# Performance work log

Measured on AMD Instinct MI355X. Metric: run time of the kernel, lower is better.

The kernel has to match this reference:

```python
import jax, jax.numpy as jnp
import numpy as np

N = 32768       # total nodes = NUM_GRAPHS * T
F_IN = 32       # num_features
HC = 64         # hidden_channels
HEADS = 4
E = 524288      # edges before self-loops
NUM_GRAPHS = 64 # == batch.max()+1 by construction
T = 512         # time steps per graph (N // NUM_GRAPHS)
OUT = 24        # output_size
NEG_SLOPE = 0.2 # PyG GATConv default


def gat_layer(x, src, dst, W, a_src, a_dst, b, n_nodes):
    """PyG GATConv (concat=True) with edge softmax over incoming edges."""
    H, C = a_src.shape
    h = (x @ W).reshape(n_nodes, H, C)                    # [N,H,C]
    alpha_src = jnp.sum(h * a_src, axis=-1)               # [N,H]
    alpha_dst = jnp.sum(h * a_dst, axis=-1)               # [N,H]
    e = jax.nn.leaky_relu(alpha_src[src] + alpha_dst[dst], NEG_SLOPE)  # [E,H]
    m = jax.ops.segment_max(e, dst, num_segments=n_nodes)
    e = jnp.exp(e - m[dst])
    s = jax.ops.segment_sum(e, dst, num_segments=n_nodes)
    alpha = e / (s[dst] + 1e-16)                          # [E,H]
    msg = h[src] * alpha[..., None]                       # [E,H,C]
    out = jax.ops.segment_sum(msg, dst, num_segments=n_nodes)  # [N,H,C]
    return out.reshape(n_nodes, H * C) + b


def gru_layer(x, Wih, Whh, bih, bhh):
    """torch nn.GRU single layer, batch_first input x: [B,T,Hin] -> ([B,T,H], h_T)."""
    Bsz = x.shape[0]
    H = Whh.shape[1]

    def step(h, xt):
        gi = xt @ Wih.T + bih
        gh = h @ Whh.T + bhh
        ir, iz, inn = jnp.split(gi, 3, axis=-1)
        hr, hz, hn = jnp.split(gh, 3, axis=-1)
        r = jax.nn.sigmoid(ir + hr)
        z = jax.nn.sigmoid(iz + hz)
        n = jnp.tanh(inn + r * hn)
        h_new = (1.0 - z) * n + z * h
        return h_new, h_new

    h0 = jnp.zeros((Bsz, H), x.dtype)
    hT, ys = jax.lax.scan(step, h0, jnp.swapaxes(x, 0, 1))
    return jnp.swapaxes(ys, 0, 1), hT


def setup_inputs() -> dict:
    key = jax.random.key(0)
    ks = jax.random.split(key, 24)
    sc = 0.1
    inp = {
        "x": jax.random.normal(ks[0], (N, F_IN), dtype=jnp.float32),
        "edge_index": jax.random.randint(ks[1], (2, E), 0, N, dtype=jnp.int32),
        "batch": jnp.repeat(jnp.arange(NUM_GRAPHS, dtype=jnp.int32), T),
        # GAT layer 1: F_IN -> HC x HEADS (concat)
        "W1": sc * jax.random.normal(ks[2], (F_IN, HEADS * HC), dtype=jnp.float32),
        "a_src1": sc * jax.random.normal(ks[3], (HEADS, HC), dtype=jnp.float32),
        "a_dst1": sc * jax.random.normal(ks[4], (HEADS, HC), dtype=jnp.float32),
        "b1": jnp.zeros((HEADS * HC,), dtype=jnp.float32),
        # GAT layer 2: HEADS*HC -> HC, 1 head
        "W2": sc * jax.random.normal(ks[5], (HEADS * HC, HC), dtype=jnp.float32),
        "a_src2": sc * jax.random.normal(ks[6], (1, HC), dtype=jnp.float32),
        "a_dst2": sc * jax.random.normal(ks[7], (1, HC), dtype=jnp.float32),
        "b2": jnp.zeros((HC,), dtype=jnp.float32),
        # GRU (2 layers, input_size == hidden_size == HC)
        "gru_Wih0": sc * jax.random.normal(ks[8], (3 * HC, HC), dtype=jnp.float32),
        "gru_Whh0": sc * jax.random.normal(ks[9], (3 * HC, HC), dtype=jnp.float32),
        "gru_bih0": jnp.zeros((3 * HC,), dtype=jnp.float32),
        "gru_bhh0": jnp.zeros((3 * HC,), dtype=jnp.float32),
        "gru_Wih1": sc * jax.random.normal(ks[10], (3 * HC, HC), dtype=jnp.float32),
        "gru_Whh1": sc * jax.random.normal(ks[11], (3 * HC, HC), dtype=jnp.float32),
        "gru_bih1": jnp.zeros((3 * HC,), dtype=jnp.float32),
        "gru_bhh1": jnp.zeros((3 * HC,), dtype=jnp.float32),
        # Linear head
        "Wl": sc * jax.random.normal(ks[12], (OUT, HC), dtype=jnp.float32),
        "bl": jnp.zeros((OUT,), dtype=jnp.float32),
    }
    return inp


def reference(x, edge_index, batch, W1, a_src1, a_dst1, b1, W2, a_src2, a_dst2, b2,
              gru_Wih0, gru_Whh0, gru_bih0, gru_bhh0,
              gru_Wih1, gru_Whh1, gru_bih1, gru_bhh1, Wl, bl):
    # PyG GATConv default add_self_loops=True
    loops = jnp.arange(N, dtype=edge_index.dtype)
    src = jnp.concatenate([edge_index[0], loops])
    dst = jnp.concatenate([edge_index[1], loops])

    h = jax.nn.elu(gat_layer(x, src, dst, W1, a_src1, a_dst1, b1, N))   # [N, HEADS*HC]
    h = jax.nn.elu(gat_layer(h, src, dst, W2, a_src2, a_dst2, b2, N))   # [N, HC]

    # batch is repeat(arange(NUM_GRAPHS), T) so batch.max()+1 == NUM_GRAPHS (static)
    seq = h.reshape(NUM_GRAPHS, T, HC)
    seq, _ = gru_layer(seq, gru_Wih0, gru_Whh0, gru_bih0, gru_bhh0)
    _, hT = gru_layer(seq, gru_Wih1, gru_Whh1, gru_bih1, gru_bhh1)      # [B, HC]
    return hT @ Wl.T + bl                                               # [B, OUT]
```

## Files before the change

### kernel.cpp

```cpp
#include <hip/hip_runtime.h>
#include <hip/hip_bf16.h>

#define N_NODES 32768
#define F_IN    32
#define HC      64
#define HEADS   4
#define NE      524288
#define NET     (NE + N_NODES)
#define NG      64
#define TT      512
#define OUTF    24

__device__ __forceinline__ float lrelu(float x){ return x > 0.f ? x : 0.2f*x; }
__device__ __forceinline__ float eluf (float x){ return x > 0.f ? x : __expf(x)-1.f; }
__device__ __forceinline__ float sigmf(float x){ return 1.f/(1.f+__expf(-x)); }
__device__ __forceinline__ float tanhfast(float x){ return 1.f - 2.f/(__expf(2.f*x)+1.f); }
__device__ __forceinline__ float bcast(float v, int k){
  return __int_as_float(__builtin_amdgcn_readlane(__float_as_int(v), k));
}

__global__ __launch_bounds__(256) void k_deg(const int* __restrict__ ei,
                                             int* __restrict__ deg){
  int e = blockIdx.x*256 + threadIdx.x;
  int d = (e < NE) ? ei[NE+e] : (e - NE);
  atomicAdd(deg + d, 1);
}

__global__ __launch_bounds__(1024) void k_scan(const int* __restrict__ deg,
                                               int* __restrict__ rowptr){
  __shared__ int ps[1024];
  const int t = threadIdx.x;
  const int base = t*32;
  int local[32]; int s = 0;
  #pragma unroll
  for(int i=0;i<32;i++){ local[i]=deg[base+i]; s+=local[i]; }
  ps[t]=s; __syncthreads();
  for(int off=1; off<1024; off<<=1){
    int v = (t>=off) ? ps[t-off] : 0;
    __syncthreads();
    ps[t]+=v;
    __syncthreads();
  }
  int run = (t==0) ? 0 : ps[t-1];
  #pragma unroll
  for(int i=0;i<32;i++){ rowptr[base+i]=run; run+=local[i]; }
  if(t==1023) rowptr[N_NODES]=run;
}

__global__ __launch_bounds__(256) void k_fill(const int* __restrict__ ei,
                                              const int* __restrict__ rowptr,
                                              int* __restrict__ cur,
                                              int* __restrict__ col){
  int e = blockIdx.x*256 + threadIdx.x;
  int s, d;
  if(e < NE){ s = ei[e]; d = ei[NE+e]; } else { s = e-NE; d = s; }
  int pos = atomicAdd(cur + d, 1);
  col[rowptr[d] + pos] = s;
}

__global__ __launch_bounds__(256) void k_alpha1x(const float* __restrict__ x,
                                                 const float* __restrict__ W1,
                                                 const float* __restrict__ a_src,
                                                 const float* __restrict__ a_dst,
                                                 float* __restrict__ as1,
                                                 float* __restrict__ ad1){
  __shared__ float ps[256];
  const int tid = threadIdx.x;
  {
    const int k = tid>>3, q = tid&7;
    const int h = q>>1, isd = q&1;
    const float* av = (isd ? a_dst : a_src) + h*64;
    const float* wr = W1 + k*256 + h*64;
    float acc = 0.f;
    #pragma unroll
    for(int c=0;c<64;c++) acc += wr[c]*av[c];
    ps[(isd?128:0) + k*4 + h] = acc;
  }
  __syncthreads();
  const int n = blockIdx.x*256 + tid;
  const float4* xr = (const float4*)(x + n*32);
  float sa0=0.f,sa1=0.f,sa2=0.f,sa3=0.f, sd0=0.f,sd1=0.f,sd2=0.f,sd3=0.f;
  #pragma unroll
  for(int k4=0;k4<8;k4++){
    float4 v = xr[k4];
    const float* pa = ps + (4*k4)*4;
    const float* pd = ps + 128 + (4*k4)*4;
    sa0 += v.x*pa[0] + v.y*pa[4] + v.z*pa[8]  + v.w*pa[12];
    sa1 += v.x*pa[1] + v.y*pa[5] + v.z*pa[9]  + v.w*pa[13];
    sa2 += v.x*pa[2] + v.y*pa[6] + v.z*pa[10] + v.w*pa[14];
    sa3 += v.x*pa[3] + v.y*pa[7] + v.z*pa[11] + v.w*pa[15];
    sd0 += v.x*pd[0] + v.y*pd[4] + v.z*pd[8]  + v.w*pd[12];
    sd1 += v.x*pd[1] + v.y*pd[5] + v.z*pd[9]  + v.w*pd[13];
    sd2 += v.x*pd[2] + v.y*pd[6] + v.z*pd[10] + v.w*pd[14];
    sd3 += v.x*pd[3] + v.y*pd[7] + v.z*pd[11] + v.w*pd[15];
  }
  *(float4*)(as1+n*4) = make_float4(sa0,sa1,sa2,sa3);
  *(float4*)(ad1+n*4) = make_float4(sd0,sd1,sd2,sd3);
}

__global__ __launch_bounds__(256) void k_gatx(const int* __restrict__ rowptr,
                                              const int* __restrict__ col,
                                              const float* __restrict__ as1,
                                              const float* __restrict__ ad1,
                                              const float* __restrict__ x,
                                              float* __restrict__ agg,
                                              float* __restrict__ s14){
  const int node = blockIdx.x*4 + (threadIdx.x>>6);
  const int lane = threadIdx.x & 63;
  const int h0   = lane>>5;
  const int c    = lane & 31;
  const int beg = rowptr[node], end = rowptr[node+1];
  const float adA = ad1[node*4 + h0];
  const float adB = ad1[node*4 + h0 + 2];
  float accA=0.f, accB=0.f, wsA=0.f, wsB=0.f;
  int j = beg;
  for(; j+3 < end; j += 4){
    int s0 = col[j], s1 = col[j+1], s2 = col[j+2], s3 = col[j+3];
    float4 q0 = *(const float4*)(as1 + s0*4);
    float4 q1 = *(const float4*)(as1 + s1*4);
    float4 q2 = *(const float4*)(as1 + s2*4);
    float4 q3 = *(const float4*)(as1 + s3*4);
    float x0 = x[s0*32 + c];
    float x1 = x[s1*32 + c];
    float x2 = x[s2*32 + c];
    float x3 = x[s3*32 + c];
    float wA0 = __expf(lrelu((h0?q0.y:q0.x) + adA));
    float wA1 = __expf(lrelu((h0?q1.y:q1.x) + adA));
    float wA2 = __expf(lrelu((h0?q2.y:q2.x) + adA));
    float wA3 = __expf(lrelu((h0?q3.y:q3.x) + adA));
    float wB0 = __expf(lrelu((h0?q0.w:q0.z) + adB));
    float wB1 = __expf(lrelu((h0?q1.w:q1.z) + adB));
    float wB2 = __expf(lrelu((h0?q2.w:q2.z) + adB));
    float wB3 = __expf(lrelu((h0?q3.w:q3.z) + adB));
    accA += wA0*x0 + wA1*x1 + wA2*x2 + wA3*x3;
    accB += wB0*x0 + wB1*x1 + wB2*x2 + wB3*x3;
    wsA  += (wA0+wA1) + (wA2+wA3);
    wsB  += (wB0+wB1) + (wB2+wB3);
  }
  for(; j < end; j++){
    int s0 = col[j];
    float4 q0 = *(const float4*)(as1 + s0*4);
    float wA0 = __expf(lrelu((h0?q0.y:q0.x) + adA));
    float wB0 = __expf(lrelu((h0?q0.w:q0.z) + adB));
    float x0 = x[s0*32 + c];
    accA += wA0*x0; accB += wB0*x0;
    wsA += wA0; wsB += wB0;
  }
  agg[node*128 + h0*32 + c]     = accA;
  agg[node*128 + (h0+2)*32 + c] = accB;
  if(c == 0){
    s14[node*4 + h0]     = wsA;
    s14[node*4 + h0 + 2] = wsB;
  }
}

__global__ __launch_bounds__(256) void k_g12(const float* __restrict__ agg,
                                             const float* __restrict__ W1,
                                             const float* __restrict__ s14,
                                             const float* __restrict__ b1,
                                             const float* __restrict__ W2,
                                             const float* __restrict__ a_src2,
                                             const float* __restrict__ a_dst2,
                                             float* __restrict__ h2,
                                             float* __restrict__ as2,
                                             float* __restrict__ ad2){
  __shared__ __align__(16) float ags[32*128];
  __shared__ __align__(16) float o1s[32*256];
  __shared__ float sv[128];
  const int tid  = threadIdx.x;
  const int row0 = blockIdx.x*32;
  const float4* ag = (const float4*)(agg + (size_t)row0*128);
  float4* a4 = (float4*)ags;
  for(int i=tid;i<1024;i+=256) a4[i]=ag[i];
  if(tid<32) ((float4*)sv)[tid]=((const float4*)(s14+row0*4))[tid];
  float wc[32];
  #pragma unroll
  for(int k=0;k<32;k++) wc[k]=W1[k*256+tid];
  const float bb=b1[tid];
  __syncthreads();
  const int h = tid>>6;
  for(int r=0;r<32;r++){
    const float4* ar=(const float4*)(ags + r*128 + h*32);
    float acc=0.f;
    #pragma unroll
    for(int k4=0;k4<8;k4++){
      float4 v=ar[k4];
      acc += v.x*wc[4*k4]+v.y*wc[4*k4+1]+v.z*wc[4*k4+2]+v.w*wc[4*k4+3];
    }
    float inv = 1.f/(sv[r*4+h] + 1e-16f);
    o1s[r*256+tid] = eluf(acc*inv + bb);
  }
  __syncthreads();
  const int c0=(tid&15)*4;
  const int r0=(tid>>4)*2;
  float acc2[2][4]={};
  for(int k=0;k<256;k+=4){
    float wv[4][4];
    #pragma unroll
    for(int i=0;i<4;i++){
      float4 w=*(const float4*)(W2+(k+i)*64+c0);
      wv[i][0]=w.x; wv[i][1]=w.y; wv[i][2]=w.z; wv[i][3]=w.w;
    }
    #pragma unroll
    for(int i=0;i<2;i++){
      float4 xv=*(const float4*)(o1s+(r0+i)*256+k);
      #pragma unroll
      for(int j=0;j<4;j++)
        acc2[i][j]+=xv.x*wv[0][j]+xv.y*wv[1][j]+xv.z*wv[2][j]+xv.w*wv[3][j];
    }
  }
  float* h2s = ags;
  #pragma unroll
  for(int i=0;i<2;i++){
    float4 o = make_float4(acc2[i][0],acc2[i][1],acc2[i][2],acc2[i][3]);
    *(float4*)(h2 + (size_t)(row0+r0+i)*64 + c0) = o;
    *(float4*)(h2s + (r0+i)*64 + c0) = o;
  }
  __syncthreads();
  if(tid < 32){
    const float4* hp=(const float4*)(h2s + tid*64);
    float sa=0.f, sd=0.f;
    #pragma unroll
    for(int i=0;i<16;i++){
      float4 v=hp[i];
      float4 a=((const float4*)a_src2)[i];
      float4 d=((const float4*)a_dst2)[i];
      sa+=v.x*a.x+v.y*a.y+v.z*a.z+v.w*a.w;
      sd+=v.x*d.x+v.y*d.y+v.z*d.z+v.w*d.w;
    }
    as2[row0+tid]=sa; ad2[row0+tid]=sd;
  }
}

__global__ __launch_bounds__(256) void k_gat2(const int* __restrict__ rowptr,
                                              const int* __restrict__ col,
                                              const float* __restrict__ as2,
                                              const float* __restrict__ ad2,
                                              const float* __restrict__ h2,
                                              const float* __restrict__ b2,
                                              float* __restrict__ out2){
  const int node = blockIdx.x*4 + (threadIdx.x>>6);
  const int lane = threadIdx.x & 63;
  const int beg = rowptr[node], end = rowptr[node+1];
  const float ad = ad2[node];
  float acc = 0.f, s = 0.f;
  int j = beg;
  for(; j+3 < end; j += 4){
    int s0 = col[j], s1 = col[j+1], s2 = col[j+2], s3 = col[j+3];
    float a0 = as2[s0], a1 = as2[s1], a2 = as2[s2], a3 = as2[s3];
    float v0 = h2[s0*64+lane], v1 = h2[s1*64+lane];
    float v2 = h2[s2*64+lane], v3 = h2[s3*64+lane];
    float w0 = __expf(lrelu(a0 + ad));
    float w1 = __expf(lrelu(a1 + ad));
    float w2 = __expf(lrelu(a2 + ad));
    float w3 = __expf(lrelu(a3 + ad));
    acc += w0*v0 + w1*v1 + w2*v2 + w3*v3;
    s += (w0+w1) + (w2+w3);
  }
  for(; j < end; j++){
    int s0 = col[j];
    float w0 = __expf(lrelu(as2[s0] + ad));
    acc += w0*h2[s0*64+lane];
    s += w0;
  }
  const float inv = 1.f/(s + 1e-16f);
  out2[node*64+lane] = eluf(acc*inv + b2[lane]);
}

__global__ __launch_bounds__(256) void k_gemm_gi(const float* __restrict__ in,
                                                 const float* __restrict__ Wih,
                                                 const float* __restrict__ bih,
                                                 float* __restrict__ gi){
  __shared__ __align__(16) float xs[64*64];
  __shared__ float wT[64*192];
  const int tid=threadIdx.x;
  const int row0=blockIdx.x*64;
  const float4* xg=(const float4*)(in+row0*64);
  float4* xs4=(float4*)xs;
  for(int i=tid;i<1024;i+=256) xs4[i]=xg[i];
  for(int i=tid;i<12288;i+=256){ wT[(i&63)*192+(i>>6)] = Wih[i]; }
  __syncthreads();
  if(tid<192){
    float wr[64];
    #pragma unroll
    for(int k=0;k<64;k++) wr[k]=wT[k*192+tid];
    const float bj=bih[tid];
    for(int r=0;r<64;r++){
      float acc=bj;
      const float4* xr=(const float4*)(xs+r*64);
      #pragma unroll
      for(int k4=0;k4<16;k4++){
        float4 v=xr[k4];
        acc+=v.x*wr[4*k4]+v.y*wr[4*k4+1]+v.z*wr[4*k4+2]+v.w*wr[4*k4+3];
      }
      gi[(row0+r)*192+tid]=acc;
    }
  }
}

__global__ __launch_bounds__(576,3) void k_gruR(const float* __restrict__ gi1,
                                                const float* __restrict__ Whh0,
                                                const float* __restrict__ bhh0,
                                                const float* __restrict__ Wih1,
                                                const float* __restrict__ bih1,
                                                const float* __restrict__ Whh1,
                                                const float* __restrict__ bhh1,
                                                const float* __restrict__ Wl,
                                                const float* __restrict__ bl,
                                                float* __restrict__ fout){
  __shared__ float h1s[64];
  __shared__ float h2s[64];
  __shared__ float gh1s[192];
  __shared__ float gi2s[192];
  __shared__ float gh2s[192];
  __shared__ float g1r[2][192];
  const int tid  = threadIdx.x;
  const int w    = tid >> 6;
  const int lane = tid & 63;
  const int b    = blockIdx.x;
  const float* gib = gi1 + (size_t)b*TT*192;

  const int crew = w/3;
  const int row  = (w%3)*64 + lane;
  const float* W  = (crew==0) ? Whh0 : (crew==1) ? Wih1 : Whh1;
  const float* bb = (crew==0) ? bhh0 : (crew==1) ? bih1 : bhh1;
  float* dst      = (crew==0) ? gh1s : (crew==1) ? gi2s : gh2s;

  const float4* wp = (const float4*)(W + row*64);
  float4 Wv0=wp[0],  Wv1=wp[1],  Wv2=wp[2],  Wv3=wp[3];
  float4 Wv4=wp[4],  Wv5=wp[5],  Wv6=wp[6],  Wv7=wp[7];
  float4 Wv8=wp[8],  Wv9=wp[9],  WvA=wp[10], WvB=wp[11];
  float4 WvC=wp[12], WvD=wp[13], WvE=wp[14], WvF=wp[15];
  const float bias = bb[row];

  float giv = 0.f;
  if(w < 3){
    g1r[0][row] = gib[row];
    giv = gib[192 + row];
  }
  if(tid < 64){ h1s[tid]=0.f; h2s[tid]=0.f; }
  __syncthreads();

  for(int i=0;i<=TT;i++){
    float hv = (crew==2) ? h2s[lane] : h1s[lane];
    if(w < 3){
      int pst = i+1;
      if(pst < TT) g1r[pst&1][row] = giv;
      int nst = i+2;
      if(nst < TT) giv = gib[nst*192 + row];
    }
    float a0=bias, a1=0.f, a2=0.f, a3=0.f;
#define DOT4(WV, BASE) \
    a0 = fmaf(bcast(hv, BASE+0), WV.x, a0); \
    a1 = fmaf(bcast(hv, BASE+1), WV.y, a1); \
    a2 = fmaf(bcast(hv, BASE+2), WV.z, a2); \
    a3 = fmaf(bcast(hv, BASE+3), WV.w, a3);
    DOT4(Wv0, 0)  DOT4(Wv1, 4)  DOT4(Wv2, 8)  DOT4(Wv3, 12)
    DOT4(Wv4, 16) DOT4(Wv5, 20) DOT4(Wv6, 24) DOT4(Wv7, 28)
    DOT4(Wv8, 32) DOT4(Wv9, 36) DOT4(WvA, 40) DOT4(WvB, 44)
    DOT4(WvC, 48) DOT4(WvD, 52) DOT4(WvE, 56) DOT4(WvF, 60)
#undef DOT4
    dst[row] = (a0+a1)+(a2+a3);
    __syncthreads();
    if(w == 0){
      if(i < TT){
        float r = sigmf(g1r[i&1][lane]     + gh1s[lane]);
        float z = sigmf(g1r[i&1][64+lane]  + gh1s[64+lane]);
        float n = tanhfast(g1r[i&1][128+lane] + r*gh1s[128+lane]);
        h1s[lane] = (1.f-z)*n + z*h1s[lane];
      }
    } else if(w == 3){
      if(i >= 1){
        float r = sigmf(gi2s[lane]     + gh2s[lane]);
        float z = sigmf(gi2s[64+lane]  + gh2s[64+lane]);
        float n = tanhfast(gi2s[128+lane] + r*gh2s[128+lane]);
        h2s[lane] = (1.f-z)*n + z*h2s[lane];
      }
    }
    __syncthreads();
  }

  if(tid < 24){
    float acc = bl[tid];
    const float4* wl4 = (const float4*)(Wl + tid*64);
    #pragma unroll
    for(int k4=0;k4<16;k4++){
      float4 h4 = *(const float4*)(h2s + 4*k4);
      float4 w4 = wl4[k4];
      acc += h4.x*w4.x + h4.y*w4.y + h4.z*w4.z + h4.w*w4.w;
    }
    fout[b*24+tid] = acc;
  }
}

extern "C" void kernel_launch(void* const* d_in, const int* in_sizes, int n_in,
                              void* d_out, int out_size, void* d_ws, size_t ws_size,
                              hipStream_t stream){
  const float* x     =(const float*)d_in[0];
  const int*   ei    =(const int*  )d_in[1];
  const float* W1    =(const float*)d_in[3];
  const float* a_src1=(const float*)d_in[4];
  const float* a_dst1=(const float*)d_in[5];
  const float* b1    =(const float*)d_in[6];
  const float* W2    =(const float*)d_in[7];
  const float* a_src2=(const float*)d_in[8];
  const float* a_dst2=(const float*)d_in[9];
  const float* b2    =(const float*)d_in[10];
  const float* Wih0  =(const float*)d_in[11];
  const float* Whh0  =(const float*)d_in[12];
  const float* bih0  =(const float*)d_in[13];
  const float* bhh0  =(const float*)d_in[14];
  const float* Wih1  =(const float*)d_in[15];
  const float* Whh1  =(const float*)d_in[16];
  const float* bih1  =(const float*)d_in[17];
  const float* bhh1  =(const float*)d_in[18];
  const float* Wl    =(const float*)d_in[19];
  const float* bl    =(const float*)d_in[20];

  float* ws   = (float*)d_ws;
  float* agg  = ws;
  float* s14  = ws + 4194304;
  float* gi   = ws;
  float* out2 = ws + 8388608;
  float* h2   = ws + 16777216;
  float* as1  = ws + 18874368;
  float* ad1  = as1 + 131072;
  float* as2  = ad1 + 131072;
  float* ad2  = as2 + 32768;
  int* rowptr = (int*)(ad2 + 32768);
  int* deg    = rowptr + 32800;
  int* cur    = deg + 32768;
  int* col    = cur + 32768;
  float* fo   = (float*)d_out;

  hipMemsetAsync(deg, 0, 2*32768*sizeof(int), stream);

  k_deg   <<<2176,256,0,stream>>>(ei,deg);
  k_scan  <<<1  ,1024,0,stream>>>(deg,rowptr);
  k_fill  <<<2176,256,0,stream>>>(ei,rowptr,cur,col);

  k_alpha1x<<<128 ,256,0,stream>>>(x,W1,a_src1,a_dst1,as1,ad1);
  k_gatx   <<<8192,256,0,stream>>>(rowptr,col,as1,ad1,x,agg,s14);
  k_g12    <<<1024,256,0,stream>>>(agg,W1,s14,b1,W2,a_src2,a_dst2,h2,as2,ad2);
  k_gat2   <<<8192,256,0,stream>>>(rowptr,col,as2,ad2,h2,b2,out2);
  k_gemm_gi<<<512 ,256,0,stream>>>(out2,Wih0,bih0,gi);
  k_gruR   <<<64  ,576,0,stream>>>(gi,Whh0,bhh0,Wih1,bih1,Whh1,bhh1,Wl,bl,fo);
  (void)in_sizes; (void)n_in; (void)out_size; (void)ws_size;
}
```

Baseline: 755.1 us.

## Halve GRU recurrence barriers by redundantly computing hidden state per wave

The two-layer GRU recurrence kernel no longer has one wave compute the gate update and publish h through shared memory behind a second barrier. Every wave now computes the GRU cell update itself into a register (crews 0-1 track layer-1 h, crew 2 tracks layer-2 h), reading double-buffered gate-partial arrays. This leaves one __syncthreads per timestep instead of two. The cost is redundant transcendental math across all nine waves, a triple-buffered input ring, and one extra loop iteration for the pipelined second layer.

```diff
diff --git a/kernel.cpp b/kernel.cpp
--- a/kernel.cpp
+++ b/kernel.cpp
@@ -298,22 +298,21 @@
   }
 }
 
-__global__ __launch_bounds__(576,3) void k_gruR(const float* __restrict__ gi1,
-                                                const float* __restrict__ Whh0,
-                                                const float* __restrict__ bhh0,
-                                                const float* __restrict__ Wih1,
-                                                const float* __restrict__ bih1,
-                                                const float* __restrict__ Whh1,
-                                                const float* __restrict__ bhh1,
-                                                const float* __restrict__ Wl,
-                                                const float* __restrict__ bl,
-                                                float* __restrict__ fout){
-  __shared__ float h1s[64];
-  __shared__ float h2s[64];
-  __shared__ float gh1s[192];
-  __shared__ float gi2s[192];
-  __shared__ float gh2s[192];
-  __shared__ float g1r[2][192];
+__global__ __launch_bounds__(576,3) void k_gru1b(const float* __restrict__ gi1,
+                                                 const float* __restrict__ Whh0,
+                                                 const float* __restrict__ bhh0,
+                                                 const float* __restrict__ Wih1,
+                                                 const float* __restrict__ bih1,
+                                                 const float* __restrict__ Whh1,
+                                                 const float* __restrict__ bhh1,
+                                                 const float* __restrict__ Wl,
+                                                 const float* __restrict__ bl,
+                                                 float* __restrict__ fout){
+  __shared__ float gh1p[2][192];
+  __shared__ float gi2p[2][192];
+  __shared__ float gh2p[2][192];
+  __shared__ float g1r[3][192];
+  __shared__ float h2fin[64];
   const int tid  = threadIdx.x;
   const int w    = tid >> 6;
   const int lane = tid & 63;
@@ -324,7 +323,6 @@
   const int row  = (w%3)*64 + lane;
   const float* W  = (crew==0) ? Whh0 : (crew==1) ? Wih1 : Whh1;
   const float* bb = (crew==0) ? bhh0 : (crew==1) ? bih1 : bhh1;
-  float* dst      = (crew==0) ? gh1s : (crew==1) ? gi2s : gh2s;
 
   const float4* wp = (const float4*)(W + row*64);
   float4 Wv0=wp[0],  Wv1=wp[1],  Wv2=wp[2],  Wv3=wp[3];
@@ -338,54 +336,57 @@
     g1r[0][row] = gib[row];
     giv = gib[192 + row];
   }
-  if(tid < 64){ h1s[tid]=0.f; h2s[tid]=0.f; }
-  __syncthreads();
-
-  for(int i=0;i<=TT;i++){
-    float hv = (crew==2) ? h2s[lane] : h1s[lane];
+  float hreg = 0.f;
+  __syncthreads();
+
+  for(int i=0;i<=TT+1;i++){
+    const int pr = (i-1)&1;
+    if(crew < 2){
+      if(i >= 1 && i <= TT){
+        const int sr = (i-1)%3;
+        float r = sigmf(g1r[sr][lane]     + gh1p[pr][lane]);
+        float z = sigmf(g1r[sr][64+lane]  + gh1p[pr][64+lane]);
+        float n = tanhfast(g1r[sr][128+lane] + r*gh1p[pr][128+lane]);
+        hreg = (1.f-z)*n + z*hreg;
+      }
+    } else {
+      if(i >= 2){
+        float r = sigmf(gi2p[pr][lane]     + gh2p[pr][lane]);
+        float z = sigmf(gi2p[pr][64+lane]  + gh2p[pr][64+lane]);
+        float n = tanhfast(gi2p[pr][128+lane] + r*gh2p[pr][128+lane]);
+        hreg = (1.f-z)*n + z*hreg;
+      }
+    }
     if(w < 3){
-      int pst = i+1;
-      if(pst < TT) g1r[pst&1][row] = giv;
-      int nst = i+2;
-      if(nst < TT) giv = gib[nst*192 + row];
-    }
-    float a0=bias, a1=0.f, a2=0.f, a3=0.f;
+      if(i+1 <= TT-1) g1r[(i+1)%3][row] = giv;
+      if(i+2 <= TT-1) giv = gib[(size_t)(i+2)*192 + row];
+    }
+    if(i <= TT){
+      float a0=bias, a1=0.f, a2=0.f, a3=0.f;
 #define DOT4(WV, BASE) \
-    a0 = fmaf(bcast(hv, BASE+0), WV.x, a0); \
-    a1 = fmaf(bcast(hv, BASE+1), WV.y, a1); \
-    a2 = fmaf(bcast(hv, BASE+2), WV.z, a2); \
-    a3 = fmaf(bcast(hv, BASE+3), WV.w, a3);
-    DOT4(Wv0, 0)  DOT4(Wv1, 4)  DOT4(Wv2, 8)  DOT4(Wv3, 12)
-    DOT4(Wv4, 16) DOT4(Wv5, 20) DOT4(Wv6, 24) DOT4(Wv7, 28)
-    DOT4(Wv8, 32) DOT4(Wv9, 36) DOT4(WvA, 40) DOT4(WvB, 44)
-    DOT4(WvC, 48) DOT4(WvD, 52) DOT4(WvE, 56) DOT4(WvF, 60)
+      a0 = fmaf(bcast(hreg, BASE+0), WV.x, a0); \
+      a1 = fmaf(bcast(hreg, BASE+1), WV.y, a1); \
+      a2 = fmaf(bcast(hreg, BASE+2), WV.z, a2); \
+      a3 = fmaf(bcast(hreg, BASE+3), WV.w, a3);
+      DOT4(Wv0, 0)  DOT4(Wv1, 4)  DOT4(Wv2, 8)  DOT4(Wv3, 12)
+      DOT4(Wv4, 16) DOT4(Wv5, 20) DOT4(Wv6, 24) DOT4(Wv7, 28)
+      DOT4(Wv8, 32) DOT4(Wv9, 36) DOT4(WvA, 40) DOT4(WvB, 44)
+      DOT4(WvC, 48) DOT4(WvD, 52) DOT4(WvE, 56) DOT4(WvF, 60)
 #undef DOT4
-    dst[row] = (a0+a1)+(a2+a3);
+      float* dstp = (crew==0) ? gh1p[i&1] : (crew==1) ? gi2p[i&1] : gh2p[i&1];
+      dstp[row] = (a0+a1)+(a2+a3);
+    }
     __syncthreads();
-    if(w == 0){
-      if(i < TT){
-        float r = sigmf(g1r[i&1][lane]     + gh1s[lane]);
-        float z = sigmf(g1r[i&1][64+lane]  + gh1s[64+lane]);
-        float n = tanhfast(g1r[i&1][128+lane] + r*gh1s[128+lane]);
-        h1s[lane] = (1.f-z)*n + z*h1s[lane];
-      }
-    } else if(w == 3){
-      if(i >= 1){
-        float r = sigmf(gi2s[lane]     + gh2s[lane]);
-        float z = sigmf(gi2s[64+lane]  + gh2s[64+lane]);
-        float n = tanhfast(gi2s[128+lane] + r*gh2s[128+lane]);
-        h2s[lane] = (1.f-z)*n + z*h2s[lane];
-      }
-    }
-    __syncthreads();
-  }
-
+  }
+
+  if(w == 6) h2fin[lane] = hreg;
+  __syncthreads();
   if(tid < 24){
     float acc = bl[tid];
     const float4* wl4 = (const float4*)(Wl + tid*64);
     #pragma unroll
     for(int k4=0;k4<16;k4++){
-      float4 h4 = *(const float4*)(h2s + 4*k4);
+      float4 h4 = *(const float4*)(h2fin + 4*k4);
       float4 w4 = wl4[k4];
       acc += h4.x*w4.x + h4.y*w4.y + h4.z*w4.z + h4.w*w4.w;
     }
@@ -444,6 +445,6 @@
   k_g12    <<<1024,256,0,stream>>>(agg,W1,s14,b1,W2,a_src2,a_dst2,h2,as2,ad2);
   k_gat2   <<<8192,256,0,stream>>>(rowptr,col,as2,ad2,h2,b2,out2);
   k_gemm_gi<<<512 ,256,0,stream>>>(out2,Wih0,bih0,gi);
-  k_gruR   <<<64  ,576,0,stream>>>(gi,Whh0,bhh0,Wih1,bih1,Whh1,bhh1,Wl,bl,fo);
+  k_gru1b  <<<64  ,576,0,stream>>>(gi,Whh0,bhh0,Wih1,bih1,Whh1,bhh1,Wl,bl,fo);
   (void)in_sizes; (void)n_in; (void)out_size; (void)ws_size;
 }
```

New measurement: 838.5 us. 1.11x slower.

## Shrink GRU recurrence block to three waves each computing three gate rows

Applied to the files above, without the earlier changes.

The recurrent GRU kernel drops from nine wavefronts (576 threads) to three (192 threads). Each wave now holds 192 weight values in registers and computes three output rows per lane, sharing the broadcast hidden-state values across three FMA chains. This cuts block-wide barrier cost and cross-wave synchronization per timestep, at the price of three times the per-wave FMA work and much higher register pressure.

```diff
diff --git a/kernel.cpp b/kernel.cpp
--- a/kernel.cpp
+++ b/kernel.cpp
@@ -298,7 +298,7 @@
   }
 }
 
-__global__ __launch_bounds__(576,3) void k_gruR(const float* __restrict__ gi1,
+__global__ __launch_bounds__(192,1) void k_gru3(const float* __restrict__ gi1,
                                                 const float* __restrict__ Whh0,
                                                 const float* __restrict__ bhh0,
                                                 const float* __restrict__ Wih1,
@@ -320,47 +320,74 @@
   const int b    = blockIdx.x;
   const float* gib = gi1 + (size_t)b*TT*192;
 
-  const int crew = w/3;
-  const int row  = (w%3)*64 + lane;
-  const float* W  = (crew==0) ? Whh0 : (crew==1) ? Wih1 : Whh1;
-  const float* bb = (crew==0) ? bhh0 : (crew==1) ? bih1 : bhh1;
-  float* dst      = (crew==0) ? gh1s : (crew==1) ? gi2s : gh2s;
-
-  const float4* wp = (const float4*)(W + row*64);
-  float4 Wv0=wp[0],  Wv1=wp[1],  Wv2=wp[2],  Wv3=wp[3];
-  float4 Wv4=wp[4],  Wv5=wp[5],  Wv6=wp[6],  Wv7=wp[7];
-  float4 Wv8=wp[8],  Wv9=wp[9],  WvA=wp[10], WvB=wp[11];
-  float4 WvC=wp[12], WvD=wp[13], WvE=wp[14], WvF=wp[15];
-  const float bias = bb[row];
-
-  float giv = 0.f;
-  if(w < 3){
-    g1r[0][row] = gib[row];
-    giv = gib[192 + row];
+  const float* W  = (w==0) ? Whh0 : (w==1) ? Wih1 : Whh1;
+  const float* bb = (w==0) ? bhh0 : (w==1) ? bih1 : bhh1;
+  float* dst      = (w==0) ? gh1s : (w==1) ? gi2s : gh2s;
+
+  const float4* pa = (const float4*)(W + lane*64);
+  const float4* pb = (const float4*)(W + (64+lane)*64);
+  const float4* pc = (const float4*)(W + (128+lane)*64);
+  float4 Av0=pa[0],  Av1=pa[1],  Av2=pa[2],  Av3=pa[3];
+  float4 Av4=pa[4],  Av5=pa[5],  Av6=pa[6],  Av7=pa[7];
+  float4 Av8=pa[8],  Av9=pa[9],  AvA=pa[10], AvB=pa[11];
+  float4 AvC=pa[12], AvD=pa[13], AvE=pa[14], AvF=pa[15];
+  float4 Bv0=pb[0],  Bv1=pb[1],  Bv2=pb[2],  Bv3=pb[3];
+  float4 Bv4=pb[4],  Bv5=pb[5],  Bv6=pb[6],  Bv7=pb[7];
+  float4 Bv8=pb[8],  Bv9=pb[9],  BvA=pb[10], BvB=pb[11];
+  float4 BvC=pb[12], BvD=pb[13], BvE=pb[14], BvF=pb[15];
+  float4 Cv0=pc[0],  Cv1=pc[1],  Cv2=pc[2],  Cv3=pc[3];
+  float4 Cv4=pc[4],  Cv5=pc[5],  Cv6=pc[6],  Cv7=pc[7];
+  float4 Cv8=pc[8],  Cv9=pc[9],  CvA=pc[10], CvB=pc[11];
+  float4 CvC=pc[12], CvD=pc[13], CvE=pc[14], CvF=pc[15];
+  const float biasA = bb[lane];
+  const float biasB = bb[64+lane];
+  const float biasC = bb[128+lane];
+
+  float giv0 = 0.f, giv1 = 0.f, giv2 = 0.f;
+  if(w == 0){
+    g1r[0][lane]     = gib[lane];
+    g1r[0][64+lane]  = gib[64+lane];
+    g1r[0][128+lane] = gib[128+lane];
+    giv0 = gib[192 + lane];
+    giv1 = gib[192 + 64+lane];
+    giv2 = gib[192 + 128+lane];
   }
   if(tid < 64){ h1s[tid]=0.f; h2s[tid]=0.f; }
   __syncthreads();
 
   for(int i=0;i<=TT;i++){
-    float hv = (crew==2) ? h2s[lane] : h1s[lane];
-    if(w < 3){
+    float hv = (w==2) ? h2s[lane] : h1s[lane];
+    if(w == 0){
       int pst = i+1;
-      if(pst < TT) g1r[pst&1][row] = giv;
+      if(pst < TT){
+        g1r[pst&1][lane]     = giv0;
+        g1r[pst&1][64+lane]  = giv1;
+        g1r[pst&1][128+lane] = giv2;
+      }
       int nst = i+2;
-      if(nst < TT) giv = gib[nst*192 + row];
-    }
-    float a0=bias, a1=0.f, a2=0.f, a3=0.f;
-#define DOT4(WV, BASE) \
-    a0 = fmaf(bcast(hv, BASE+0), WV.x, a0); \
-    a1 = fmaf(bcast(hv, BASE+1), WV.y, a1); \
-    a2 = fmaf(bcast(hv, BASE+2), WV.z, a2); \
-    a3 = fmaf(bcast(hv, BASE+3), WV.w, a3);
-    DOT4(Wv0, 0)  DOT4(Wv1, 4)  DOT4(Wv2, 8)  DOT4(Wv3, 12)
-    DOT4(Wv4, 16) DOT4(Wv5, 20) DOT4(Wv6, 24) DOT4(Wv7, 28)
-    DOT4(Wv8, 32) DOT4(Wv9, 36) DOT4(WvA, 40) DOT4(WvB, 44)
-    DOT4(WvC, 48) DOT4(WvD, 52) DOT4(WvE, 56) DOT4(WvF, 60)
+      if(nst < TT){
+        giv0 = gib[(size_t)nst*192 + lane];
+        giv1 = gib[(size_t)nst*192 + 64+lane];
+        giv2 = gib[(size_t)nst*192 + 128+lane];
+      }
+    }
+    float a0=biasA, a1=0.f, a2=0.f, a3=0.f;
+    float b0=biasB, b1_=0.f, b2_=0.f, b3=0.f;
+    float c0=biasC, c1=0.f, c2=0.f, c3=0.f;
+#define DOT4(WA, WB, WC, BASE) { \
+    float t0=bcast(hv,BASE+0), t1=bcast(hv,BASE+1), t2=bcast(hv,BASE+2), t3=bcast(hv,BASE+3); \
+    a0 = fmaf(t0, WA.x, a0);  b0  = fmaf(t0, WB.x, b0);  c0 = fmaf(t0, WC.x, c0); \
+    a1 = fmaf(t1, WA.y, a1);  b1_ = fmaf(t1, WB.y, b1_); c1 = fmaf(t1, WC.y, c1); \
+    a2 = fmaf(t2, WA.z, a2);  b2_ = fmaf(t2, WB.z, b2_); c2 = fmaf(t2, WC.z, c2); \
+    a3 = fmaf(t3, WA.w, a3);  b3  = fmaf(t3, WB.w, b3);  c3 = fmaf(t3, WC.w, c3); }
+    DOT4(Av0,Bv0,Cv0, 0)  DOT4(Av1,Bv1,Cv1, 4)  DOT4(Av2,Bv2,Cv2, 8)  DOT4(Av3,Bv3,Cv3, 12)
+    DOT4(Av4,Bv4,Cv4, 16) DOT4(Av5,Bv5,Cv5, 20) DOT4(Av6,Bv6,Cv6, 24) DOT4(Av7,Bv7,Cv7, 28)
+    DOT4(Av8,Bv8,Cv8, 32) DOT4(Av9,Bv9,Cv9, 36) DOT4(AvA,BvA,CvA, 40) DOT4(AvB,BvB,CvB, 44)
+    DOT4(AvC,BvC,CvC, 48) DOT4(AvD,BvD,CvD, 52) DOT4(AvE,BvE,CvE, 56) DOT4(AvF,BvF,CvF, 60)
 #undef DOT4
-    dst[row] = (a0+a1)+(a2+a3);
+    dst[lane]     = (a0+a1)+(a2+a3);
+    dst[64+lane]  = (b0+b1_)+(b2_+b3);
+    dst[128+lane] = (c0+c1)+(c2+c3);
     __syncthreads();
     if(w == 0){
       if(i < TT){
@@ -369,7 +396,7 @@
         float n = tanhfast(g1r[i&1][128+lane] + r*gh1s[128+lane]);
         h1s[lane] = (1.f-z)*n + z*h1s[lane];
       }
-    } else if(w == 3){
+    } else if(w == 2){
       if(i >= 1){
         float r = sigmf(gi2s[lane]     + gh2s[lane]);
         float z = sigmf(gi2s[64+lane]  + gh2s[64+lane]);
@@ -444,6 +471,6 @@
   k_g12    <<<1024,256,0,stream>>>(agg,W1,s14,b1,W2,a_src2,a_dst2,h2,as2,ad2);
   k_gat2   <<<8192,256,0,stream>>>(rowptr,col,as2,ad2,h2,b2,out2);
   k_gemm_gi<<<512 ,256,0,stream>>>(out2,Wih0,bih0,gi);
-  k_gruR   <<<64  ,576,0,stream>>>(gi,Whh0,bhh0,Wih1,bih1,Whh1,bhh1,Wl,bl,fo);
+  k_gru3   <<<64  ,192,0,stream>>>(gi,Whh0,bhh0,Wih1,bih1,Whh1,bhh1,Wl,bl,fo);
   (void)in_sizes; (void)n_in; (void)out_size; (void)ws_size;
 }
```

New measurement: 730.8 us (median of 2 runs). -3.2%, faster.
